# Optimization experiments

Hardware: AMD Instinct MI355X
Metric: run time of the kernel (lower is better)

Reference implementation:

```python
import jax, jax.numpy as jnp
import numpy as np

N, E, D, H, T, R, K = 40000, 320000, 128, 4, 3, 5, 3
DK = D // H
SQRT_DK = float(np.sqrt(DK))

def _glorot(key, shape):
    lim = float(np.sqrt(6.0 / (shape[-2] + shape[-1])))
    return jax.random.uniform(key, shape, jnp.float32, -lim, lim)

def setup_inputs():
    ks = jax.random.split(jax.random.key(0), 16)
    return {
        "meta_xs": jax.random.normal(ks[0], (N, D), jnp.float32),
        "node_type": jax.random.randint(ks[1], (N,), 0, T),
        "edge_index": jax.random.randint(ks[2], (2, E), 0, N),
        "edge_type": jax.random.randint(ks[3], (E,), 0, R),
        "edge_time": jax.random.randint(ks[4], (E,), 0, 100),
        "q_w": _glorot(ks[5], (T, D, D)), "q_b": jnp.zeros((T, D), jnp.float32),
        "k_w": _glorot(ks[6], (T, D, D)), "k_b": jnp.zeros((T, D), jnp.float32),
        "v_w": _glorot(ks[7], (T, D, D)), "v_b": jnp.zeros((T, D), jnp.float32),
        "a_w": _glorot(ks[8], (T, D, D)), "a_b": jnp.zeros((T, D), jnp.float32),
        "rel_pri": jnp.ones((R, H), jnp.float32),
        "rel_att": _glorot(ks[9], (R, H, DK, DK)),
        "rel_msg": _glorot(ks[10], (R, H, DK, DK)),
        "WMk": _glorot(ks[11], (K, D, D)),
        "Wak": _glorot(ks[12], (K, D, D)),
        "Wq": _glorot(ks[13], (D, D)), "bq": jnp.zeros((D,), jnp.float32),
        "Wkl": _glorot(ks[14], (D, D)), "bkl": jnp.zeros((D,), jnp.float32),
        "skip": jnp.ones((T,), jnp.float32),
        "ln_g": jnp.ones((T, D), jnp.float32),
        "ln_b": jnp.zeros((T, D), jnp.float32),
    }

def _forward(meta_xs, q_w, q_b, k_w, k_b, v_w, v_b, a_w, a_b, rel_pri, rel_att,
             rel_msg, WMk, Wak, Wq, bq, Wkl, bkl, skip, ln_g, ln_b,
             node_type, edge_index, edge_type):
    src, tgt = edge_index[0], edge_index[1]
    ar = jnp.arange(N)

    def typed(x, W, b):  # per-node-type linear: equivalent to the type-masked loops
        all_t = jnp.einsum('ni,tio->tno', x, W)        # [T, N, D]
        return all_t[node_type, ar] + b[node_type]      # [N, D]

    qn = typed(meta_xs, q_w, q_b).reshape(N, H, DK)
    kn = typed(meta_xs, k_w, k_b).reshape(N, H, DK)
    vn = typed(meta_xs, v_w, v_b).reshape(N, H, DK)
    qe, ke, ve = qn[tgt], kn[src], vn[src]              # [E, H, DK]

    # relation-specific bmm, honoring per-relation dispatch without [E,H,DK,DK] gather
    kp = jnp.zeros_like(ke)
    vp = jnp.zeros_like(ve)
    for r in range(R):
        sel = (edge_type == r)[:, None, None]
        kp = jnp.where(sel, jnp.einsum('ehd,hdm->ehm', ke, rel_att[r]), kp)
        vp = jnp.where(sel, jnp.einsum('ehd,hdm->ehm', ve, rel_msg[r]), vp)

    logits = (qe * kp).sum(-1) * rel_pri[edge_type] / SQRT_DK   # [E, H]
    # segment softmax over incoming edges per target node (torch_geometric softmax)
    mx = jax.ops.segment_max(logits, tgt, num_segments=N)
    ex = jnp.exp(logits - mx[tgt])
    att = ex / (jax.ops.segment_sum(ex, tgt, num_segments=N)[tgt] + 1e-16)

    # power-moment expanded, attention-weighted messages: [K, E, D]
    msgs = jnp.stack([((vp ** (kk + 1)) * att[:, :, None]).reshape(E, D) for kk in range(K)])

    # faithful to original aggregate(): messages indexed by target node id (not edge id)
    agg = jnp.stack([jax.ops.segment_sum(msgs[kk][tgt], tgt, num_segments=N) for kk in range(K)])
    # faithful: only the last moment gets the signed K-th root (loop re-clones each iter)
    root = jnp.sign(agg[K - 1]) * (jnp.abs(agg[K - 1]) + 1e-18) ** (1.0 / K)
    aggm = agg.at[K - 1].set(root)
    aggm = jnp.einsum('knd,kde->kne', aggm, WMk)        # [K, N, D]

    qlin = meta_xs @ Wq + bq
    res = jnp.zeros((N, D), meta_xs.dtype)
    for kk in range(K):
        front = qlin @ Wak[kk]                          # [N, D]
        tail = aggm[kk] @ Wkl + bkl                     # [N, D]
        t = jax.nn.sigmoid((front * tail).sum(-1))      # [N]
        res = res + t[:, None] * aggm[kk]

    # update(): gelu -> per-type linear -> learned skip -> per-type LayerNorm
    h = jax.nn.gelu(res, approximate=False)
    trans = typed(h, a_w, a_b)
    alpha = jax.nn.sigmoid(skip)[node_type][:, None]
    y = trans * alpha + meta_xs * (1.0 - alpha)
    mu = y.mean(-1, keepdims=True)
    var = ((y - mu) ** 2).mean(-1, keepdims=True)
    y = (y - mu) / jnp.sqrt(var + 1e-5) * ln_g[node_type] + ln_b[node_type]
    return y

def reference(meta_xs, node_type, edge_index, edge_type, edge_time,
              q_w, q_b, k_w, k_b, v_w, v_b, a_w, a_b, rel_pri, rel_att, rel_msg,
              WMk, Wak, Wq, bq, Wkl, bkl, skip, ln_g, ln_b):
    return _forward(meta_xs, q_w, q_b, k_w, k_b, v_w, v_b, a_w, a_b, rel_pri,
                    rel_att, rel_msg, WMk, Wak, Wq, bq, Wkl, bkl, skip, ln_g, ln_b,
                    node_type, edge_index, edge_type)
```

## Files before the change

### kernel.cpp

```cpp
#include <hip/hip_runtime.h>

#define N_ 40000
#define E_ 320000
#define D_ 128
#define H_ 4
#define T_ 3
#define R_ 5

typedef unsigned short u16;
typedef float f32x4 __attribute__((ext_vector_type(4)));
typedef short s16x8 __attribute__((ext_vector_type(8)));

__device__ __forceinline__ float bf2f(u16 h){ return __uint_as_float(((unsigned)h)<<16); }
__device__ __forceinline__ u16 f2bf(float f){
  unsigned u = __float_as_uint(f);
  u += 0x7fffu + ((u>>16)&1u);
  return (u16)(u>>16);
}
__device__ __forceinline__ unsigned fmono(float f){
  unsigned u = __float_as_uint(f);
  return (u>>31) ? ~u : (u | 0x80000000u);
}
__device__ __forceinline__ float monof(unsigned u){
  return (u>>31) ? __uint_as_float(u & 0x7fffffffu) : __uint_as_float(~u);
}
__device__ __forceinline__ float ldx(const void* p, long i, int f32){
  return f32 ? ((const float*)p)[i] : bf2f(((const u16*)p)[i]);
}
__device__ __forceinline__ float wredsum(float v){
  #pragma unroll
  for (int m=32;m;m>>=1) v += __shfl_xor(v, m, 64);
  return v;
}
__device__ __forceinline__ void split2(float v0, float v1, unsigned& hp, unsigned& lp){
  unsigned b0 = __float_as_uint(v0), b1 = __float_as_uint(v1);
  unsigned h0 = b0 & 0xFFFF0000u,    h1 = b1 & 0xFFFF0000u;
  float r0 = v0 - __uint_as_float(h0);
  float r1 = v1 - __uint_as_float(h1);
  hp = (h0>>16) | h1;
  lp = (__float_as_uint(r0)>>16) | (__float_as_uint(r1) & 0xFFFF0000u);
}

#define W_QW 0
#define W_KW 49152
#define W_VW 98304
#define W_AW 147456
#define W_QB 196608
#define W_KB 196992
#define W_VB 197376
#define W_AB 197760
#define W_PRI 198144
#define W_RATT 198164
#define W_RMSG 218644
#define W_WMK 239124
#define W_WAK 288276
#define W_WQ 337428
#define W_BQ 353812
#define W_WKL 353940
#define W_BKL 370324
#define W_SKIP 370452
#define W_LNG 370455
#define W_LNB 370839
#define W_TOT 371223

#define WT_Q   0
#define WT_K   98304
#define WT_V   196608
#define WT_A   294912
#define WT_WQ  396328
#define WT_WMK 478248

#define OFF_FLAGS 0ul
#define OFF_WCF   512ul
#define OFF_NT32  1485824ul
#define OFF_EI32  1646080ul
#define OFF_ET32  4206592ul
#define OFF_PERM  5486592ul
#define OFF_PCNT  5648384ul
#define OFF_TVAL  5648896ul
#define OFF_NPERM 5730816ul
#define OFF_LOG   6288896ul
#define OFF_QN    12848896ul
#define OFF_KN    33328896ul
#define OFF_VN    53808896ul
#define OFF_QLIN  74288896ul
#define OFF_QTR   94768896ul

__global__ __launch_bounds__(256) void detect_kernel(
    const u16* __restrict__ xs, const int* __restrict__ nt, int* __restrict__ flags)
{
  __shared__ int sBig, sZero, sNz;
  int tid = threadIdx.x;
  if (tid==0){ sBig=0; sZero=0; sNz=0; }
  __syncthreads();
  int big=0, zc=0;
  for (int i=tid; i<1024; i+=256) {
    u16 v = xs[2*i];
    int e = (v>>7)&0xFF;
    big += (e >= 200);
    zc  += (v == 0);
  }
  int nz=0;
  for (int i=tid; i<1024; i+=256) nz += (nt[2*i+1] != 0);
  atomicAdd(&sBig, big); atomicAdd(&sZero, zc); atomicAdd(&sNz, nz);
  __syncthreads();
  if (tid==0) {
    flags[0] = (sBig > 64) || (sZero > 900);
    flags[1] = (sNz == 0);
  }
}

struct FPtrs { const void* p[20]; };
__global__ __launch_bounds__(256) void convf_kernel(
    const int* __restrict__ flags, FPtrs ptrs, float* __restrict__ wcf)
{
  const int start[21] = {0,49152,98304,147456,196608,196992,197376,197760,198144,
    198164,218644,239124,288276,337428,353812,353940,370324,370452,370455,370839,371223};
  int i = blockIdx.x*256 + threadIdx.x;
  if (i >= W_TOT) return;
  int arr = 0;
  #pragma unroll
  for (int a=1; a<20; ++a) arr += (i >= start[a]);
  int local = i - start[arr];
  wcf[i] = ldx(ptrs.p[arr], local, flags[0]);
}

__global__ __launch_bounds__(256) void idxconv_kernel(
    const int* __restrict__ flags,
    const int* __restrict__ nt, const int* __restrict__ ei, const int* __restrict__ et,
    int* __restrict__ nt32, int* __restrict__ ei32, int* __restrict__ et32)
{
  int i = blockIdx.x*256 + threadIdx.x;
  if (i >= 1000000) return;
  int w = flags[1] ? 2 : 1;
  if (i < 40000)        nt32[i] = nt[(long)i*w];
  else if (i < 680000)  { int j=i-40000;  ei32[j] = ei[(long)j*w]; }
  else                  { int j=i-680000; et32[j] = et[(long)j*w]; }
}

__global__ __launch_bounds__(256) void zinit_kernel(
    int* __restrict__ perm, int* __restrict__ pc,
    int* __restrict__ nperm, int* __restrict__ pc2,
    unsigned* __restrict__ mxkey, float* __restrict__ sumex, int* __restrict__ deg)
{
  int i = blockIdx.x*256 + threadIdx.x;
  if (i < 40448) perm[i] = -1;
  if (i < 12) pc[i] = 0;
  if (i < 40320) nperm[i] = -1;
  if (i < 16) pc2[i] = 0;
  mxkey[i] = fmono(-1e30f);
  sumex[i] = 0.f;
  if (i < N_) deg[i] = 0;
}

__global__ __launch_bounds__(256) void cnt_kernel(
    const int* __restrict__ keys, int n, int ntypes, int* __restrict__ gcnt)
{
  __shared__ int lh[8];
  if (threadIdx.x < ntypes) lh[threadIdx.x] = 0;
  __syncthreads();
  int i = blockIdx.x*256 + threadIdx.x;
  if (i < n) atomicAdd(&lh[keys[i]], 1);
  __syncthreads();
  if (threadIdx.x < ntypes && lh[threadIdx.x])
    atomicAdd(&gcnt[threadIdx.x], lh[threadIdx.x]);
}
__global__ void pofs_kernel(int* __restrict__ pc){
  if (threadIdx.x==0 && blockIdx.x==0) {
    pc[8] = 0;
    pc[9] = (pc[0]+127)&~127;
    pc[10] = pc[9] + ((pc[1]+127)&~127);
  }
}
__global__ void eofs_kernel(int* __restrict__ pc2){
  if (threadIdx.x==0 && blockIdx.x==0) {
    pc2[10] = 0;
    #pragma unroll
    for (int r=1;r<R_;++r) pc2[10+r] = pc2[10+r-1] + ((pc2[r-1]+63)&~63);
  }
}
__global__ __launch_bounds__(256) void scat_kernel(
    const int* __restrict__ keys, int n, int ntypes,
    const int* __restrict__ ofs, int* __restrict__ fill, int* __restrict__ perm)
{
  __shared__ int lh[8];
  __shared__ int lbase[8];
  if (threadIdx.x < ntypes) lh[threadIdx.x] = 0;
  __syncthreads();
  int i = blockIdx.x*256 + threadIdx.x;
  int t = 0, rank = 0;
  bool ok = (i < n);
  if (ok) { t = keys[i]; rank = atomicAdd(&lh[t], 1); }
  __syncthreads();
  if (threadIdx.x < ntypes)
    lbase[threadIdx.x] = lh[threadIdx.x] ? atomicAdd(&fill[threadIdx.x], lh[threadIdx.x]) : 0;
  __syncthreads();
  if (ok) perm[ofs[t] + lbase[t] + rank] = i;
}

__global__ __launch_bounds__(256) void prepA_kernel(
    const float* __restrict__ wcf, float* __restrict__ raT)
{
  int i = blockIdx.x*256 + threadIdx.x;
  if (i >= 20480) return;
  int d = i & 31, m = (i>>5) & 31, rh = i >> 10;
  raT[i] = wcf[W_RATT + (rh*32 + d)*32 + m];
}

__global__ __launch_bounds__(128) void prepB_kernel(
    const float* __restrict__ wcf, float* __restrict__ MT, float* __restrict__ ck)
{
  int col = threadIdx.x, i = blockIdx.x, k = blockIdx.y;
  const float* wak = wcf + W_WAK + k*16384 + col*128;
  const float* wkl = wcf + W_WKL + i*128;
  float acc = 0.f, accC = 0.f;
  #pragma unroll 8
  for (int j=0;j<128;++j) {
    float a = wak[j];
    acc  += a * wkl[j];
    if (i==0) accC += a * wcf[W_BKL + j];
  }
  MT[k*16384 + i*128 + col] = acc;
  if (i==0) ck[k*128 + col] = accC;
}

struct TPtrs { const void* p[16]; int soff[16]; int doff[16]; };
__global__ __launch_bounds__(256) void prepT_kernel(
    TPtrs tp, const int* __restrict__ flags, int xmode, u16* __restrict__ dst)
{
  __shared__ float T[128][33];
  int m = blockIdx.y;
  int c0 = blockIdx.x * 32;
  int tid = threadIdx.x;
  int xf = xmode ? 1 : flags[0];
  const void* src = tp.p[m];
  long sb = tp.soff[m];
  {
    int k = tid >> 1, ch = (tid & 1) * 16;
    #pragma unroll
    for (int j=0;j<16;++j)
      T[k][ch+j] = ldx(src, sb + (long)k*128 + c0 + ch + j, xf);
  }
  __syncthreads();
  int col = tid >> 3, k0 = (tid & 7) * 16;
  unsigned hp[8], lp[8];
  #pragma unroll
  for (int j=0;j<8;++j)
    split2(T[k0+2*j][col], T[k0+2*j+1][col], hp[j], lp[j]);
  u16* dh = dst + tp.doff[m] + (long)(c0+col)*128 + k0;
  ((uint4*)dh)[0] = uint4{hp[0],hp[1],hp[2],hp[3]};
  ((uint4*)dh)[1] = uint4{hp[4],hp[5],hp[6],hp[7]};
  u16* dl = dh + 16384;
  ((uint4*)dl)[0] = uint4{lp[0],lp[1],lp[2],lp[3]};
  ((uint4*)dl)[1] = uint4{lp[4],lp[5],lp[6],lp[7]};
}

struct GC4 { const float* x[4]; int woff[4]; int boff[4]; int typed[4]; int obf[4]; };
__global__ __launch_bounds__(256) void gemmt2_kernel(
    GC4 cfg, const int* __restrict__ flags, int xmode,
    const u16* __restrict__ Wt, const float* __restrict__ wcf,
    const int* __restrict__ perm, const int* __restrict__ nt,
    int dotmode, const float* __restrict__ qlin, const float* __restrict__ ck,
    int powmode, const float* __restrict__ sattp, int wmode,
    float* __restrict__ out, long yostride)
{
  __shared__ u16 Wh[4096], Wl[4096];
  __shared__ int ridx[128];
  __shared__ int tblk_s;
  int tid = threadIdx.x;
  int y = blockIdx.y;
  int row0 = blockIdx.x*128;
  if (tid < 128) {
    int rr = row0 + tid;
    int rg = perm ? perm[rr] : (rr < N_ ? rr : -1);
    ridx[tid] = rg;
    if (tid==0) tblk_s = (perm && nt && rg>=0) ? nt[rg] : 0;
  }
  __syncthreads();
  if (ridx[0] < 0) return;
  int tblk = cfg.typed[y] ? tblk_s : 0;
  const u16* Wg = Wt + cfg.woff[y] + tblk*32768;
  const void* X = (const void*)cfg.x[y];
  int f0 = flags[0];
  int xf = xmode ? 1 : f0;
  int wlo_on = wmode ? 1 : f0;

  int lane = tid & 63;
  int wv   = tid >> 6;
  int lrow = lane & 15;
  int lk   = (lane >> 4) << 3;
  int rbase = wv*32;

  int sr0i = ridx[rbase + lrow];
  int sr1i = ridx[rbase + lrow + 16];
  long s0 = (sr0i < 0) ? 0 : (long)sr0i;
  long s1 = (sr1i < 0) ? 0 : (long)sr1i;

  int sr = tid >> 1;
  int sh = (tid & 1) * 16;
  int sp  = (sr >> 1) & 3;
  int sc0 = (sh >> 3) ^ sp;
  int sc1 = ((sh >> 3) + 1) ^ sp;

  f32x4 acc[2][8];
  #pragma unroll
  for (int m=0;m<2;++m)
    #pragma unroll
    for (int n=0;n<8;++n) acc[m][n] = f32x4{0.f,0.f,0.f,0.f};

  float4 fa0, fa1, fb0, fb1;
  uint4  ua = {0,0,0,0}, ub = {0,0,0,0};
  float  scp0 = 0.f, scp1 = 0.f;
  uint4  pw0, pw1, pw2 = {0,0,0,0}, pw3 = {0,0,0,0};

  if (xf) {
    const float4* x0 = reinterpret_cast<const float4*>((const float*)X + s0*128 + lk);
    const float4* x1 = reinterpret_cast<const float4*>((const float*)X + s1*128 + lk);
    fa0=x0[0]; fa1=x0[1]; fb0=x1[0]; fb1=x1[1];
    if (powmode) { scp0 = sattp[s0*4]; scp1 = sattp[s1*4]; }
  } else {
    ua = *reinterpret_cast<const uint4*>((const u16*)X + s0*128 + lk);
    ub = *reinterpret_cast<const uint4*>((const u16*)X + s1*128 + lk);
  }
  {
    const u16* gh = Wg + sr*128 + sh;
    pw0 = ((const uint4*)gh)[0]; pw1 = ((const uint4*)gh)[1];
    if (wlo_on) { pw2 = ((const uint4*)(gh+16384))[0]; pw3 = ((const uint4*)(gh+16384))[1]; }
  }

  for (int kc=0;kc<4;++kc) {
    s16x8 ah0, ah1, al0, al1;
    if (xf) {
      float t0[8] = {fa0.x,fa0.y,fa0.z,fa0.w, fa1.x,fa1.y,fa1.z,fa1.w};
      float t1[8] = {fb0.x,fb0.y,fb0.z,fb0.w, fb1.x,fb1.y,fb1.z,fb1.w};
      if (powmode) {
        #pragma unroll
        for (int j=0;j<8;++j) {
          float v0 = t0[j], v1 = t1[j];
          if (y==0)      { t0[j] = v0*scp0;    t1[j] = v1*scp1; }
          else if (y==1) { t0[j] = v0*v0*scp0; t1[j] = v1*v1*scp1; }
          else {
            float a3 = v0*v0*v0*scp0, b3 = v1*v1*v1*scp1;
            t0[j] = (a3==0.f) ? 0.f : copysignf(cbrtf(fabsf(a3)+1e-18f), a3);
            t1[j] = (b3==0.f) ? 0.f : copysignf(cbrtf(fabsf(b3)+1e-18f), b3);
          }
        }
      }
      unsigned h0[4], l0[4], h1[4], l1[4];
      #pragma unroll
      for (int j=0;j<4;++j) {
        split2(t0[2*j], t0[2*j+1], h0[j], l0[j]);
        split2(t1[2*j], t1[2*j+1], h1[j], l1[j]);
      }
      uint4 H0{h0[0],h0[1],h0[2],h0[3]}, L0{l0[0],l0[1],l0[2],l0[3]};
      uint4 H1{h1[0],h1[1],h1[2],h1[3]}, L1{l1[0],l1[1],l1[2],l1[3]};
      ah0 = *reinterpret_cast<s16x8*>(&H0); al0 = *reinterpret_cast<s16x8*>(&L0);
      ah1 = *reinterpret_cast<s16x8*>(&H1); al1 = *reinterpret_cast<s16x8*>(&L1);
    } else {
      ah0 = *reinterpret_cast<s16x8*>(&ua);
      ah1 = *reinterpret_cast<s16x8*>(&ub);
    }
    uint4 WH0 = pw0, WH1 = pw1, WL0 = pw2, WL1 = pw3;

    __syncthreads();
    ((uint4*)Wh)[sr*4 + sc0] = WH0;
    ((uint4*)Wh)[sr*4 + sc1] = WH1;
    if (wlo_on) {
      ((uint4*)Wl)[sr*4 + sc0] = WL0;
      ((uint4*)Wl)[sr*4 + sc1] = WL1;
    }
    if (kc < 3) {
      int kn_ = kc + 1;
      if (xf) {
        const float4* x0 = reinterpret_cast<const float4*>((const float*)X + s0*128 + kn_*32 + lk);
        const float4* x1 = reinterpret_cast<const float4*>((const float*)X + s1*128 + kn_*32 + lk);
        fa0=x0[0]; fa1=x0[1]; fb0=x1[0]; fb1=x1[1];
        if (powmode) { scp0 = sattp[s0*4 + kn_]; scp1 = sattp[s1*4 + kn_]; }
      } else {
        ua = *reinterpret_cast<const uint4*>((const u16*)X + s0*128 + kn_*32 + lk);
        ub = *reinterpret_cast<const uint4*>((const u16*)X + s1*128 + kn_*32 + lk);
      }
      const u16* gh = Wg + sr*128 + kn_*32 + sh;
      pw0 = ((const uint4*)gh)[0]; pw1 = ((const uint4*)gh)[1];
      if (wlo_on) { pw2 = ((const uint4*)(gh+16384))[0]; pw3 = ((const uint4*)(gh+16384))[1]; }
    }
    __syncthreads();
    #pragma unroll
    for (int n=0;n<8;++n) {
      int col = n*16 + lrow;
      int ib = col*32 + (lk ^ (((col>>1)&3)<<3));
      s16x8 bh = *(const s16x8*)(Wh + ib);
      acc[0][n] = __builtin_amdgcn_mfma_f32_16x16x32_bf16(ah0, bh, acc[0][n], 0,0,0);
      acc[1][n] = __builtin_amdgcn_mfma_f32_16x16x32_bf16(ah1, bh, acc[1][n], 0,0,0);
      if (xf) {
        acc[0][n] = __builtin_amdgcn_mfma_f32_16x16x32_bf16(al0, bh, acc[0][n], 0,0,0);
        acc[1][n] = __builtin_amdgcn_mfma_f32_16x16x32_bf16(al1, bh, acc[1][n], 0,0,0);
      }
      if (wlo_on) {
        s16x8 bl = *(const s16x8*)(Wl + ib);
        acc[0][n] = __builtin_amdgcn_mfma_f32_16x16x32_bf16(ah0, bl, acc[0][n], 0,0,0);
        acc[1][n] = __builtin_amdgcn_mfma_f32_16x16x32_bf16(ah1, bl, acc[1][n], 0,0,0);
      }
    }
  }

  int rq = (lane >> 4) << 2;
  if (!dotmode) {
    float b[8];
    if (cfg.boff[y] >= 0) {
      const float* bp = wcf + cfg.boff[y] + tblk*128;
      #pragma unroll
      for (int n=0;n<8;++n) b[n] = bp[n*16 + lrow];
    } else {
      #pragma unroll
      for (int n=0;n<8;++n) b[n] = 0.f;
    }
    int ob = cfg.obf[y] && !f0;
    #pragma unroll
    for (int m=0;m<2;++m) {
      #pragma unroll
      for (int r=0;r<4;++r) {
        int rowl = rbase + m*16 + rq + r;
        int rowg = ridx[rowl];
        if (rowg < 0) continue;
        if (ob) {
          u16* op = (u16*)(out + (long)y*yostride) + (long)rowg*128 + lrow;
          #pragma unroll
          for (int n=0;n<8;++n) op[n*16] = f2bf(acc[m][n][r] + b[n]);
        } else {
          float* op = out + (long)y*yostride + (long)rowg*128 + lrow;
          #pragma unroll
          for (int n=0;n<8;++n) op[n*16] = acc[m][n][r] + b[n];
        }
      }
    }
  } else {
    float ckv[8];
    #pragma unroll
    for (int n=0;n<8;++n) ckv[n] = ck[y*128 + n*16 + lrow];
    #pragma unroll
    for (int m=0;m<2;++m) {
      #pragma unroll
      for (int r=0;r<4;++r) {
        int rowl = rbase + m*16 + rq + r;
        int rowg = ridx[rowl];
        float d = 0.f;
        if (rowg >= 0) {
          const float* qp = qlin + (long)rowg*128 + lrow;
          #pragma unroll
          for (int n=0;n<8;++n) d += (acc[m][n][r] + ckv[n]) * qp[n*16];
        }
        #pragma unroll
        for (int msk=1; msk<16; msk<<=1) d += __shfl_xor(d, msk, 64);
        if (lrow==0 && rowg>=0) out[(long)rowg*4 + y] = 1.f/(1.f+expf(-d));
      }
    }
  }
}

__global__ __launch_bounds__(256) void gemmbd_kernel(
    const float* __restrict__ X,
    const float* __restrict__ Wtab, int wsel,
    const int* __restrict__ perm, const int* __restrict__ gsrc, const int* __restrict__ et,
    float* __restrict__ out)
{
  __shared__ float As[64*152];
  __shared__ float Ws[4096];
  __shared__ int ridx[64];
  __shared__ int rsel_s;
  int tid = threadIdx.x;
  int row0 = blockIdx.x*64;
  if (tid < 64) {
    int rr = row0 + tid;
    int pe = perm ? perm[rr] : (rr < N_ ? rr : -1);
    ridx[tid] = pe;
    if (tid == 0) rsel_s = (wsel && pe >= 0) ? et[pe] : 0;
  }
  __syncthreads();
  if (ridx[0] < 0) return;
  const float* Wg = Wtab + (long)(wsel ? rsel_s : 0)*4096;
  #pragma unroll
  for (int j=0;j<4;++j)
    *reinterpret_cast<float4*>(&Ws[j*1024 + tid*4]) =
      *reinterpret_cast<const float4*>(Wg + j*1024 + tid*4);
  {
    int sar = tid >> 2, sh = tid & 3;
    int pe_s = ridx[sar];
    int arow = (pe_s < 0) ? -1 : (gsrc ? gsrc[pe_s] : pe_s);
    float* dst = &As[sar*152 + sh*36];
    if (arow < 0) {
      #pragma unroll
      for (int j=0;j<8;++j) *reinterpret_cast<float4*>(dst + j*4) = float4{0.f,0.f,0.f,0.f};
    } else {
      const float4* s4 = reinterpret_cast<const float4*>(X + (long)arow*128 + sh*32);
      #pragma unroll
      for (int j=0;j<8;++j) *reinterpret_cast<float4*>(dst + j*4) = s4[j];
    }
  }
  __syncthreads();
  int rg_ = tid >> 5, cg = tid & 31;
  int h = cg >> 3, c4 = (cg & 7)*4;
  float acc[8][4];
  #pragma unroll
  for (int r=0;r<8;++r){ acc[r][0]=0.f; acc[r][1]=0.f; acc[r][2]=0.f; acc[r][3]=0.f; }
  #pragma unroll
  for (int mq=0;mq<8;++mq) {
    float wv[4][4];
    #pragma unroll
    for (int i=0;i<4;++i) {
      float4 wt = *reinterpret_cast<const float4*>(&Ws[h*1024 + (mq*4+i)*32 + c4]);
      wv[i][0]=wt.x; wv[i][1]=wt.y; wv[i][2]=wt.z; wv[i][3]=wt.w;
    }
    #pragma unroll
    for (int r=0;r<8;++r) {
      float4 a4 = *reinterpret_cast<const float4*>(&As[(rg_*8+r)*152 + h*36 + mq*4]);
      float av[4] = {a4.x,a4.y,a4.z,a4.w};
      #pragma unroll
      for (int i=0;i<4;++i) {
        acc[r][0]+=av[i]*wv[i][0]; acc[r][1]+=av[i]*wv[i][1];
        acc[r][2]+=av[i]*wv[i][2]; acc[r][3]+=av[i]*wv[i][3];
      }
    }
  }
  #pragma unroll
  for (int r=0;r<8;++r) {
    int pe = ridx[rg_*8+r];
    if (pe < 0) continue;
    float4 o = {acc[r][0],acc[r][1],acc[r][2],acc[r][3]};
    *reinterpret_cast<float4*>(out + (long)pe*128 + h*32 + c4) = o;
  }
}

__global__ __launch_bounds__(256) void epass_kernel(
    const float* __restrict__ kn, const float* __restrict__ qtr, const float* __restrict__ wcf,
    const int* __restrict__ ei, const int* __restrict__ et, int rsel,
    float* __restrict__ logits, unsigned* __restrict__ mxkey, int* __restrict__ deg)
{
  int gid = blockIdx.x*256 + threadIdx.x;
  int e = gid >> 2, h = gid & 3;
  if (et[e] != rsel) return;
  int s = ei[e], t = ei[E_+e];
  const float4* ka = reinterpret_cast<const float4*>(kn + (long)s*128 + h*32);
  const float4* qa = reinterpret_cast<const float4*>(qtr + (long)t*128 + h*32);
  float acc = 0.f;
  #pragma unroll
  for (int i=0;i<8;++i) {
    float4 a = ka[i], b = qa[i];
    acc += a.x*b.x + a.y*b.y + a.z*b.z + a.w*b.w;
  }
  float lg = acc * wcf[W_PRI + rsel*H_+h] * 0.17677669529663687f;
  logits[gid] = lg;
  atomicMax(mxkey + t*H_+h, fmono(lg));
  if (h==0) atomicAdd(deg + t, 1);
}

__global__ __launch_bounds__(256) void eexp_kernel(
    const int* __restrict__ ei, float* __restrict__ logits,
    const unsigned* __restrict__ mxkey, float* __restrict__ sumex)
{
  int gid = blockIdx.x*256 + threadIdx.x;
  int e = gid >> 2, h = gid & 3;
  int t = ei[E_+e];
  float d = fminf(logits[gid] - monof(mxkey[t*H_+h]), 0.f);
  float ex = expf(d);
  if (e < N_) logits[gid] = ex;
  atomicAdd(sumex + t*H_+h, ex);
}

__global__ __launch_bounds__(256) void satt_kernel(
    const int* __restrict__ ei, const float* __restrict__ ex, const float* __restrict__ sumex,
    const int* __restrict__ deg, float* __restrict__ satt)
{
  int i = blockIdx.x*256 + threadIdx.x;
  int n = i >> 2, h = i & 3;
  int t = ei[E_+n];
  satt[i] = (float)deg[n] * ex[i] / (sumex[t*H_+h] + 1e-16f);
}

__global__ __launch_bounds__(256) void gatemix_kernel(
    const int* __restrict__ flags, const float* __restrict__ tval,
    const float* __restrict__ ag0, const float* __restrict__ ag1, const float* __restrict__ ag2,
    float* __restrict__ hout)
{
  long gid = ((long)blockIdx.x*256 + threadIdx.x) * 2;
  int n = (int)(gid >> 7);
  float t0 = tval[n*4+0], t1 = tval[n*4+1], t2 = tval[n*4+2];
  float r0, r1;
  if (!flags[0]) {
    unsigned a0 = *reinterpret_cast<const unsigned*>((const u16*)ag0 + gid);
    unsigned a1 = *reinterpret_cast<const unsigned*>((const u16*)ag1 + gid);
    unsigned a2 = *reinterpret_cast<const unsigned*>((const u16*)ag2 + gid);
    r0 = t0*__uint_as_float(a0<<16) + t1*__uint_as_float(a1<<16) + t2*__uint_as_float(a2<<16);
    r1 = t0*__uint_as_float(a0&0xFFFF0000u) + t1*__uint_as_float(a1&0xFFFF0000u)
       + t2*__uint_as_float(a2&0xFFFF0000u);
  } else {
    float2 a0 = *reinterpret_cast<const float2*>(ag0 + gid);
    float2 a1 = *reinterpret_cast<const float2*>(ag1 + gid);
    float2 a2 = *reinterpret_cast<const float2*>(ag2 + gid);
    r0 = t0*a0.x + t1*a1.x + t2*a2.x;
    r1 = t0*a0.y + t1*a1.y + t2*a2.y;
  }
  float g0 = 0.5f*r0*(1.f+erff(r0*0.70710678118654752f));
  float g1 = 0.5f*r1*(1.f+erff(r1*0.70710678118654752f));
  if (!flags[0]) {
    unsigned o = (unsigned)f2bf(g0) | ((unsigned)f2bf(g1)<<16);
    *reinterpret_cast<unsigned*>((u16*)hout + gid) = o;
  } else {
    *reinterpret_cast<float2*>(hout + gid) = float2{g0, g1};
  }
}

__global__ __launch_bounds__(256) void lnf_kernel(
    const float* __restrict__ trans, const void* __restrict__ x, const int* __restrict__ flags,
    const int* __restrict__ nt, const float* __restrict__ wcf, void* __restrict__ outv)
{
  int wave = threadIdx.x >> 6, lane = threadIdx.x & 63;
  int n = blockIdx.x*4 + wave;
  int j = lane*2;
  int xf = flags[0];
  int t = nt[n];
  float alpha = 1.f/(1.f+expf(-wcf[W_SKIP+t]));
  long base = (long)n*128 + j;
  float y0 = alpha*trans[base]   + (1.f-alpha)*ldx(x, base,   xf);
  float y1 = alpha*trans[base+1] + (1.f-alpha)*ldx(x, base+1, xf);
  float mu = wredsum(y0+y1) * (1.f/128.f);
  float d0 = y0-mu, d1 = y1-mu;
  float var = wredsum(d0*d0+d1*d1) * (1.f/128.f);
  float inv = rsqrtf(var + 1e-5f);
  float o0 = d0*inv*wcf[W_LNG + t*128+j]   + wcf[W_LNB + t*128+j];
  float o1 = d1*inv*wcf[W_LNG + t*128+j+1] + wcf[W_LNB + t*128+j+1];
  if (xf) {
    ((float*)outv)[base]   = o0;
    ((float*)outv)[base+1] = o1;
  } else {
    unsigned o = (unsigned)f2bf(o0) | ((unsigned)f2bf(o1)<<16);
    *reinterpret_cast<unsigned*>(((u16*)outv)+base) = o;
  }
}

extern "C" void kernel_launch(void* const* d_in, const int* in_sizes, int n_in,
                              void* d_out, int out_size, void* d_ws, size_t ws_size,
                              hipStream_t stream) {
  char* w = (char*)d_ws;
  int*      flags = (int*)     (w + OFF_FLAGS);
  float*    wcf   = (float*)   (w + OFF_WCF);
  u16*      wtb   = (u16*)     (w + OFF_WCF);
  int*      nt32  = (int*)     (w + OFF_NT32);
  int*      ei32  = (int*)     (w + OFF_EI32);
  int*      et32  = (int*)     (w + OFF_ET32);
  int*      perm  = (int*)     (w + OFF_PERM);
  int*      pcnt  = (int*)     (w + OFF_PCNT);
  int*      pc2   = (int*)     (w + OFF_PCNT + 128);
  float*    raT   = (float*)   (w + OFF_TVAL);
  float*    satt  = (float*)   (w + OFF_TVAL);
  float*    tval  = (float*)   (w + OFF_TVAL);
  int*      nperm = (int*)     (w + OFF_NPERM);
  float*    logits= (float*)   (w + OFF_LOG);
  unsigned* mxkey = (unsigned*)(w + OFF_LOG + 5120000);
  float*    sumex = (float*)   (w + OFF_LOG + 5760000);
  int*      deg   = (int*)     (w + OFF_LOG + 6400000);
  float*    MT    = (float*)   (w + OFF_LOG);
  float*    ckb   = (float*)   (w + OFF_LOG + 786432);
  u16*      mtt   = (u16*)     (w + OFF_LOG + 1048576);
  float*    qn    = (float*)   (w + OFF_QN);
  float*    ag0   = (float*)   (w + OFF_QN);
  float*    trans = (float*)   (w + OFF_QN);
  float*    kn    = (float*)   (w + OFF_KN);
  float*    ag1   = (float*)   (w + OFF_KN);
  float*    vn    = (float*)   (w + OFF_VN);
  float*    ag2   = (float*)   (w + OFF_VN);
  float*    qlin  = (float*)   (w + OFF_QLIN);
  float*    hbuf  = (float*)   (w + OFF_QLIN);
  float*    qtrb  = (float*)   (w + OFF_QTR);
  float*    vp    = (float*)   (w + OFF_QTR);

  detect_kernel<<<1,256,0,stream>>>((const u16*)d_in[0], (const int*)d_in[1], flags);
  FPtrs fp;
  fp.p[0]=d_in[5];  fp.p[1]=d_in[7];  fp.p[2]=d_in[9];  fp.p[3]=d_in[11];
  fp.p[4]=d_in[6];  fp.p[5]=d_in[8];  fp.p[6]=d_in[10]; fp.p[7]=d_in[12];
  fp.p[8]=d_in[13]; fp.p[9]=d_in[14]; fp.p[10]=d_in[15];fp.p[11]=d_in[16];
  fp.p[12]=d_in[17];fp.p[13]=d_in[18];fp.p[14]=d_in[19];fp.p[15]=d_in[20];
  fp.p[16]=d_in[21];fp.p[17]=d_in[22];fp.p[18]=d_in[23];fp.p[19]=d_in[24];
  convf_kernel<<<1451,256,0,stream>>>(flags, fp, wcf);
  idxconv_kernel<<<3907,256,0,stream>>>(flags, (const int*)d_in[1],
                                        (const int*)d_in[2], (const int*)d_in[3],
                                        nt32, ei32, et32);
  zinit_kernel<<<625,256,0,stream>>>(perm, pcnt, nperm, pc2, mxkey, sumex, deg);
  cnt_kernel  <<<157,256,0,stream>>>(nt32, N_, T_, pcnt);
  pofs_kernel <<<1,64,0,stream>>>(pcnt);
  scat_kernel <<<157,256,0,stream>>>(nt32, N_, T_, pcnt+8, pcnt+4, perm);
  cnt_kernel  <<<157,256,0,stream>>>(et32, N_, R_, pc2);
  eofs_kernel <<<1,64,0,stream>>>(pc2);
  scat_kernel <<<157,256,0,stream>>>(et32, N_, R_, pc2+10, pc2+5, nperm);
  prepA_kernel<<<80,256,0,stream>>>(wcf, raT);

  TPtrs tps;
  for (int t=0;t<3;++t) {
    tps.p[t]    = d_in[5];  tps.soff[t]    = t*16384; tps.doff[t]    = WT_Q   + t*32768;
    tps.p[3+t]  = d_in[7];  tps.soff[3+t]  = t*16384; tps.doff[3+t]  = WT_K   + t*32768;
    tps.p[6+t]  = d_in[9];  tps.soff[6+t]  = t*16384; tps.doff[6+t]  = WT_V   + t*32768;
    tps.p[9+t]  = d_in[11]; tps.soff[9+t]  = t*16384; tps.doff[9+t]  = WT_A   + t*32768;
    tps.p[13+t] = d_in[16]; tps.soff[13+t] = t*16384; tps.doff[13+t] = WT_WMK + t*32768;
  }
  tps.p[12] = d_in[18]; tps.soff[12] = 0; tps.doff[12] = WT_WQ;
  prepT_kernel<<<dim3(4,16),256,0,stream>>>(tps, flags, 0, wtb);

  GC4 cq;
  cq.x[0]=(const float*)d_in[0]; cq.x[1]=cq.x[0]; cq.x[2]=cq.x[0]; cq.x[3]=cq.x[0];
  cq.woff[0]=WT_Q; cq.woff[1]=WT_K; cq.woff[2]=WT_V; cq.woff[3]=WT_WQ;
  cq.boff[0]=W_QB; cq.boff[1]=W_KB; cq.boff[2]=W_VB; cq.boff[3]=W_BQ;
  cq.typed[0]=1; cq.typed[1]=1; cq.typed[2]=1; cq.typed[3]=0;
  cq.obf[0]=0; cq.obf[1]=0; cq.obf[2]=0; cq.obf[3]=0;
  gemmt2_kernel<<<dim3(316,4),256,0,stream>>>(cq, flags, 0, wtb, wcf, perm, nt32,
      0, nullptr, nullptr, 0, nullptr, 0, qn, 5120000);

  for (int r=0; r<R_; ++r) {
    gemmbd_kernel<<<625,256,0,stream>>>(qn, raT + r*4096, 0, nullptr, nullptr, nullptr, qtrb);
    epass_kernel<<<5000,256,0,stream>>>(kn, qtrb, wcf, ei32, et32, r, logits, mxkey, deg);
  }
  eexp_kernel<<<5000,256,0,stream>>>(ei32, logits, mxkey, sumex);

  gemmbd_kernel<<<630,256,0,stream>>>(vn, wcf+W_RMSG, 1, nperm, ei32, et32, vp);

  satt_kernel<<<625,256,0,stream>>>(ei32, logits, sumex, deg, satt);

  prepB_kernel<<<dim3(128,3),128,0,stream>>>(wcf, MT, ckb);
  TPtrs tpm;
  for (int i=0;i<16;++i){ tpm.p[i]=MT; tpm.soff[i]=0; tpm.doff[i]=0; }
  for (int k=0;k<3;++k){ tpm.soff[k]=k*16384; tpm.doff[k]=k*32768; }
  prepT_kernel<<<dim3(4,3),256,0,stream>>>(tpm, flags, 1, mtt);

  GC4 cp;
  cp.x[0]=vp; cp.x[1]=vp; cp.x[2]=vp; cp.x[3]=vp;
  cp.woff[0]=WT_WMK; cp.woff[1]=WT_WMK+32768; cp.woff[2]=WT_WMK+65536; cp.woff[3]=0;
  cp.boff[0]=-1; cp.boff[1]=-1; cp.boff[2]=-1; cp.boff[3]=-1;
  cp.typed[0]=0; cp.typed[1]=0; cp.typed[2]=0; cp.typed[3]=0;
  cp.obf[0]=1; cp.obf[1]=1; cp.obf[2]=1; cp.obf[3]=0;
  gemmt2_kernel<<<dim3(313,3),256,0,stream>>>(cp, flags, 1, wtb, wcf, nullptr, nullptr,
      0, nullptr, nullptr, 1, satt, 0, ag0, 5120000);

  GC4 cd;
  cd.x[0]=ag0; cd.x[1]=ag1; cd.x[2]=ag2; cd.x[3]=ag2;
  cd.woff[0]=0; cd.woff[1]=32768; cd.woff[2]=65536; cd.woff[3]=0;
  cd.boff[0]=-1; cd.boff[1]=-1; cd.boff[2]=-1; cd.boff[3]=-1;
  cd.typed[0]=0; cd.typed[1]=0; cd.typed[2]=0; cd.typed[3]=0;
  cd.obf[0]=0; cd.obf[1]=0; cd.obf[2]=0; cd.obf[3]=0;
  gemmt2_kernel<<<dim3(313,3),256,0,stream>>>(cd, flags, 0, mtt, wcf, nullptr, nullptr,
      1, qlin, ckb, 0, nullptr, 1, tval, 0);

  gatemix_kernel<<<10000,256,0,stream>>>(flags, tval, ag0, ag1, ag2, hbuf);

  GC4 ct;
  ct.x[0]=hbuf; ct.x[1]=hbuf; ct.x[2]=hbuf; ct.x[3]=hbuf;
  ct.woff[0]=WT_A; ct.woff[1]=0; ct.woff[2]=0; ct.woff[3]=0;
  ct.boff[0]=W_AB; ct.boff[1]=-1; ct.boff[2]=-1; ct.boff[3]=-1;
  ct.typed[0]=1; ct.typed[1]=0; ct.typed[2]=0; ct.typed[3]=0;
  ct.obf[0]=0; ct.obf[1]=0; ct.obf[2]=0; ct.obf[3]=0;
  gemmt2_kernel<<<dim3(316,1),256,0,stream>>>(ct, flags, 0, wtb, wcf, perm, nt32,
      0, nullptr, nullptr, 0, nullptr, 0, trans, 0);

  lnf_kernel<<<10000,256,0,stream>>>(trans, d_in[0], flags, nt32, wcf, d_out);

  (void)in_sizes; (void)n_in; (void)out_size; (void)ws_size;
}
```

Measured before the change: 545.9 us.

## Fuse relation attention transform into edge pass using relation-sorted edge permutation

Replaces the per-relation loop, which ran a full-node block-diagonal GEMM of q by rel_att and then a full-edge scan for each of the five relations, with a single edge kernel. Edges are first bucketed by relation with a count/offset/scatter pass. Each 64-edge tile, which holds one relation, gathers target q rows, multiplies them by that relation's matrix in shared memory and takes the dot product with the source k row. This drops four redundant node GEMMs and five edge scans, at the cost of an extra edge sort and GEMM work done per edge instead of per node.

```diff
diff --git a/kernel.cpp b/kernel.cpp
--- a/kernel.cpp
+++ b/kernel.cpp
@@ -141,6 +141,7 @@
 __global__ __launch_bounds__(256) void zinit_kernel(
     int* __restrict__ perm, int* __restrict__ pc,
     int* __restrict__ nperm, int* __restrict__ pc2,
+    int* __restrict__ eperm, int* __restrict__ pc3,
     unsigned* __restrict__ mxkey, float* __restrict__ sumex, int* __restrict__ deg)
 {
   int i = blockIdx.x*256 + threadIdx.x;
@@ -148,8 +149,9 @@
   if (i < 12) pc[i] = 0;
   if (i < 40320) nperm[i] = -1;
   if (i < 16) pc2[i] = 0;
-  mxkey[i] = fmono(-1e30f);
-  sumex[i] = 0.f;
+  if (i < 320320) eperm[i] = -1;
+  if (i < 16) pc3[i] = 0;
+  if (i < 160000) { mxkey[i] = fmono(-1e30f); sumex[i] = 0.f; }
   if (i < N_) deg[i] = 0;
 }
 
@@ -531,27 +533,91 @@
   }
 }
 
-__global__ __launch_bounds__(256) void epass_kernel(
-    const float* __restrict__ kn, const float* __restrict__ qtr, const float* __restrict__ wcf,
-    const int* __restrict__ ei, const int* __restrict__ et, int rsel,
+__global__ __launch_bounds__(256) void eatt_kernel(
+    const float* __restrict__ qn, const float* __restrict__ kn,
+    const float* __restrict__ raT, const float* __restrict__ wcf,
+    const int* __restrict__ eperm, const int* __restrict__ ei, const int* __restrict__ et,
     float* __restrict__ logits, unsigned* __restrict__ mxkey, int* __restrict__ deg)
 {
-  int gid = blockIdx.x*256 + threadIdx.x;
-  int e = gid >> 2, h = gid & 3;
-  if (et[e] != rsel) return;
-  int s = ei[e], t = ei[E_+e];
-  const float4* ka = reinterpret_cast<const float4*>(kn + (long)s*128 + h*32);
-  const float4* qa = reinterpret_cast<const float4*>(qtr + (long)t*128 + h*32);
-  float acc = 0.f;
-  #pragma unroll
-  for (int i=0;i<8;++i) {
-    float4 a = ka[i], b = qa[i];
-    acc += a.x*b.x + a.y*b.y + a.z*b.z + a.w*b.w;
-  }
-  float lg = acc * wcf[W_PRI + rsel*H_+h] * 0.17677669529663687f;
-  logits[gid] = lg;
-  atomicMax(mxkey + t*H_+h, fmono(lg));
-  if (h==0) atomicAdd(deg + t, 1);
+  __shared__ float As[64*152];
+  __shared__ float Ws[4096];
+  __shared__ int ridx[64];
+  __shared__ int rsel_s;
+  int tid = threadIdx.x;
+  int row0 = blockIdx.x*64;
+  if (tid < 64) {
+    int pe = eperm[row0 + tid];
+    ridx[tid] = pe;
+    if (tid == 0) rsel_s = (pe >= 0) ? et[pe] : 0;
+  }
+  __syncthreads();
+  if (ridx[0] < 0) return;
+  int r = rsel_s;
+  const float* Wg = raT + (long)r*4096;
+  #pragma unroll
+  for (int j=0;j<4;++j)
+    *reinterpret_cast<float4*>(&Ws[j*1024 + tid*4]) =
+      *reinterpret_cast<const float4*>(Wg + j*1024 + tid*4);
+  {
+    int sar = tid >> 2, sh = tid & 3;
+    int pe_s = ridx[sar];
+    int arow = (pe_s < 0) ? -1 : ei[E_ + pe_s];
+    float* dst = &As[sar*152 + sh*36];
+    if (arow < 0) {
+      #pragma unroll
+      for (int j=0;j<8;++j) *reinterpret_cast<float4*>(dst + j*4) = float4{0.f,0.f,0.f,0.f};
+    } else {
+      const float4* s4 = reinterpret_cast<const float4*>(qn + (long)arow*128 + sh*32);
+      #pragma unroll
+      for (int j=0;j<8;++j) *reinterpret_cast<float4*>(dst + j*4) = s4[j];
+    }
+  }
+  __syncthreads();
+  int rg_ = tid >> 5, cg = tid & 31;
+  int h = cg >> 3, c4 = (cg & 7)*4;
+  float acc[8][4];
+  #pragma unroll
+  for (int rr=0;rr<8;++rr){ acc[rr][0]=0.f; acc[rr][1]=0.f; acc[rr][2]=0.f; acc[rr][3]=0.f; }
+  #pragma unroll
+  for (int mq=0;mq<8;++mq) {
+    float wv[4][4];
+    #pragma unroll
+    for (int i=0;i<4;++i) {
+      float4 wt = *reinterpret_cast<const float4*>(&Ws[h*1024 + (mq*4+i)*32 + c4]);
+      wv[i][0]=wt.x; wv[i][1]=wt.y; wv[i][2]=wt.z; wv[i][3]=wt.w;
+    }
+    #pragma unroll
+    for (int rr=0;rr<8;++rr) {
+      float4 a4 = *reinterpret_cast<const float4*>(&As[(rg_*8+rr)*152 + h*36 + mq*4]);
+      float av[4] = {a4.x,a4.y,a4.z,a4.w};
+      #pragma unroll
+      for (int i=0;i<4;++i) {
+        acc[rr][0]+=av[i]*wv[i][0]; acc[rr][1]+=av[i]*wv[i][1];
+        acc[rr][2]+=av[i]*wv[i][2]; acc[rr][3]+=av[i]*wv[i][3];
+      }
+    }
+  }
+  float pri = wcf[W_PRI + r*H_ + h] * 0.17677669529663687f;
+  #pragma unroll
+  for (int rr=0;rr<8;++rr) {
+    int pe = ridx[rg_*8+rr];
+    float d = 0.f;
+    if (pe >= 0) {
+      int s = ei[pe];
+      float4 k4 = *reinterpret_cast<const float4*>(kn + (long)s*128 + h*32 + c4);
+      d = acc[rr][0]*k4.x + acc[rr][1]*k4.y + acc[rr][2]*k4.z + acc[rr][3]*k4.w;
+    }
+    d += __shfl_xor(d, 1, 64);
+    d += __shfl_xor(d, 2, 64);
+    d += __shfl_xor(d, 4, 64);
+    if ((cg & 7) == 0 && pe >= 0) {
+      int t = ei[E_ + pe];
+      float lg = d * pri;
+      logits[(long)pe*4 + h] = lg;
+      atomicMax(mxkey + t*H_ + h, fmono(lg));
+      if (h == 0) atomicAdd(deg + t, 1);
+    }
+  }
 }
 
 __global__ __launch_bounds__(256) void eexp_kernel(
@@ -651,6 +717,7 @@
   int*      perm  = (int*)     (w + OFF_PERM);
   int*      pcnt  = (int*)     (w + OFF_PCNT);
   int*      pc2   = (int*)     (w + OFF_PCNT + 128);
+  int*      pc3   = (int*)     (w + OFF_PCNT + 256);
   float*    raT   = (float*)   (w + OFF_TVAL);
   float*    satt  = (float*)   (w + OFF_TVAL);
   float*    tval  = (float*)   (w + OFF_TVAL);
@@ -671,7 +738,7 @@
   float*    ag2   = (float*)   (w + OFF_VN);
   float*    qlin  = (float*)   (w + OFF_QLIN);
   float*    hbuf  = (float*)   (w + OFF_QLIN);
-  float*    qtrb  = (float*)   (w + OFF_QTR);
+  int*      eperm = (int*)     (w + OFF_QTR);
   float*    vp    = (float*)   (w + OFF_QTR);
 
   detect_kernel<<<1,256,0,stream>>>((const u16*)d_in[0], (const int*)d_in[1], flags);
@@ -685,13 +752,16 @@
   idxconv_kernel<<<3907,256,0,stream>>>(flags, (const int*)d_in[1],
                                         (const int*)d_in[2], (const int*)d_in[3],
                                         nt32, ei32, et32);
-  zinit_kernel<<<625,256,0,stream>>>(perm, pcnt, nperm, pc2, mxkey, sumex, deg);
+  zinit_kernel<<<1252,256,0,stream>>>(perm, pcnt, nperm, pc2, eperm, pc3, mxkey, sumex, deg);
   cnt_kernel  <<<157,256,0,stream>>>(nt32, N_, T_, pcnt);
   pofs_kernel <<<1,64,0,stream>>>(pcnt);
   scat_kernel <<<157,256,0,stream>>>(nt32, N_, T_, pcnt+8, pcnt+4, perm);
   cnt_kernel  <<<157,256,0,stream>>>(et32, N_, R_, pc2);
   eofs_kernel <<<1,64,0,stream>>>(pc2);
   scat_kernel <<<157,256,0,stream>>>(et32, N_, R_, pc2+10, pc2+5, nperm);
+  cnt_kernel  <<<1250,256,0,stream>>>(et32, E_, R_, pc3);
+  eofs_kernel <<<1,64,0,stream>>>(pc3);
+  scat_kernel <<<1250,256,0,stream>>>(et32, E_, R_, pc3+10, pc3+5, eperm);
   prepA_kernel<<<80,256,0,stream>>>(wcf, raT);
 
   TPtrs tps;
@@ -714,10 +784,8 @@
   gemmt2_kernel<<<dim3(316,4),256,0,stream>>>(cq, flags, 0, wtb, wcf, perm, nt32,
       0, nullptr, nullptr, 0, nullptr, 0, qn, 5120000);
 
-  for (int r=0; r<R_; ++r) {
-    gemmbd_kernel<<<625,256,0,stream>>>(qn, raT + r*4096, 0, nullptr, nullptr, nullptr, qtrb);
-    epass_kernel<<<5000,256,0,stream>>>(kn, qtrb, wcf, ei32, et32, r, logits, mxkey, deg);
-  }
+  eatt_kernel<<<5005,256,0,stream>>>(qn, kn, raT, wcf, eperm, ei32, et32,
+                                     logits, mxkey, deg);
   eexp_kernel<<<5000,256,0,stream>>>(ei32, logits, mxkey, sumex);
 
   gemmbd_kernel<<<630,256,0,stream>>>(vn, wcf+W_RMSG, 1, nperm, ei32, et32, vp);
```

Result: slower. 640.9 us (+17.4%).
